# Optimization experiments

Measured on AMD Instinct MI355X. Metric: run time of the kernel, lower is better.

The kernel has to match this reference:

```python
import jax, jax.numpy as jnp
import numpy as np

H, C = 4, 32          # num_heads, hidden_channels
NEG_ATT = 0.2         # GAT attention leaky_relu slope (PyG default)
NEG_ACT = 0.01        # F.leaky_relu default slope applied after each conv


def gat_conv(x_src, x_dst, Wsrc, Wdst, a_src, a_dst, bias, src_idx, dst_idx, n_dst):
    """One bipartite GATConv (add_self_loops=False, concat=True)."""
    hs = (x_src @ Wsrc).reshape(-1, H, C)            # [Ns,H,C]
    hd = (x_dst @ Wdst).reshape(-1, H, C)            # [Nd,H,C]
    a_s = (hs * a_src).sum(-1)                       # [Ns,H]
    a_d = (hd * a_dst).sum(-1)                       # [Nd,H]
    e = jax.nn.leaky_relu(a_s[src_idx] + a_d[dst_idx], NEG_ATT)  # [E,H]
    m = jax.ops.segment_max(e, dst_idx, num_segments=n_dst)      # [Nd,H]
    ex = jnp.exp(e - m[dst_idx])
    denom = jax.ops.segment_sum(ex, dst_idx, num_segments=n_dst)
    alpha = ex / (denom[dst_idx] + 1e-16)            # edge softmax over dst
    msg = hs[src_idx] * alpha[:, :, None]            # [E,H,C]
    out = jax.ops.segment_sum(msg, dst_idx, num_segments=n_dst)  # [Nd,H,C]
    return out.reshape(n_dst, H * C) + bias


def setup_inputs() -> dict:
    key = jax.random.key(0)
    ks = jax.random.split(key, 40)
    it = iter(range(40))
    Nu, Nm, E, D, O = 100000, 20000, 500000, 64, 64
    HC = H * C

    def rn(shape, s=0.1):
        return jax.random.normal(ks[next(it)], shape, jnp.float32) * s

    def ri(n, hi):
        return jax.random.randint(ks[next(it)], (n,), 0, hi)

    return {
        "user_ids": jnp.arange(Nu), "movie_ids": jnp.arange(Nm),
        "um_src": ri(E, Nu), "um_dst": ri(E, Nm),
        "mu_src": ri(E, Nm), "mu_dst": ri(E, Nu),
        "user_emb": rn((Nu, D)), "movie_emb": rn((Nm, D)),
        "l1_um_Wsrc": rn((D, HC)), "l1_um_Wdst": rn((D, HC)),
        "l1_um_asrc": rn((H, C)), "l1_um_adst": rn((H, C)), "l1_um_b": rn((HC,)),
        "l1_mu_Wsrc": rn((D, HC)), "l1_mu_Wdst": rn((D, HC)),
        "l1_mu_asrc": rn((H, C)), "l1_mu_adst": rn((H, C)), "l1_mu_b": rn((HC,)),
        "l2_um_W": rn((HC, HC)), "l2_um_asrc": rn((H, C)), "l2_um_adst": rn((H, C)), "l2_um_b": rn((HC,)),
        "l2_mu_W": rn((HC, HC)), "l2_mu_asrc": rn((H, C)), "l2_mu_adst": rn((H, C)), "l2_mu_b": rn((HC,)),
        "Wo": rn((HC, O)), "bo": rn((O,)),
    }


def reference(user_ids, movie_ids, um_src, um_dst, mu_src, mu_dst,
              user_emb, movie_emb,
              l1_um_Wsrc, l1_um_Wdst, l1_um_asrc, l1_um_adst, l1_um_b,
              l1_mu_Wsrc, l1_mu_Wdst, l1_mu_asrc, l1_mu_adst, l1_mu_b,
              l2_um_W, l2_um_asrc, l2_um_adst, l2_um_b,
              l2_mu_W, l2_mu_asrc, l2_mu_adst, l2_mu_b,
              Wo, bo):
    xu = user_emb[user_ids]
    xm = movie_emb[movie_ids]
    Nu, Nm = xu.shape[0], xm.shape[0]
    # layer 1 (HeteroConv sum: each dst type receives exactly one edge type here)
    hm = gat_conv(xu, xm, l1_um_Wsrc, l1_um_Wdst, l1_um_asrc, l1_um_adst, l1_um_b, um_src, um_dst, Nm)
    hu = gat_conv(xm, xu, l1_mu_Wsrc, l1_mu_Wdst, l1_mu_asrc, l1_mu_adst, l1_mu_b, mu_src, mu_dst, Nu)
    xu = jax.nn.leaky_relu(hu, NEG_ACT)
    xm = jax.nn.leaky_relu(hm, NEG_ACT)
    # layer 2 (non-bipartite in_channels int => shared lin for src and dst)
    hm = gat_conv(xu, xm, l2_um_W, l2_um_W, l2_um_asrc, l2_um_adst, l2_um_b, um_src, um_dst, Nm)
    hu = gat_conv(xm, xu, l2_mu_W, l2_mu_W, l2_mu_asrc, l2_mu_adst, l2_mu_b, mu_src, mu_dst, Nu)
    xu = jax.nn.leaky_relu(hu, NEG_ACT)
    xm = jax.nn.leaky_relu(hm, NEG_ACT)
    out_user = xu @ Wo + bo
    out_movie = xm @ Wo + bo
    return out_user, out_movie, xu, xm
```

## Files before the change

kernel.cpp:

```cpp
#include <hip/hip_runtime.h>
#include <hip/hip_bf16.h>
#include <cstdint>


#define HC 128
#define HH 4
#define NWIN 2

typedef __attribute__((ext_vector_type(8))) short bf16x8;
typedef __attribute__((ext_vector_type(4))) float f32x4;

__device__ __forceinline__ short f2bf(float f) {
    return __builtin_bit_cast(short, __float2bfloat16(f));
}
__device__ __forceinline__ float bf2f(ushort u) {
    return __builtin_bit_cast(float, ((unsigned)u) << 16);
}

struct VT { const float* W[8]; const float* a[8]; float* v[8]; };
__global__ void make_v_all_k(VT t) {
    int gid = blockIdx.x * 256 + threadIdx.x;
    int task, base;
    if (gid < 1024) { task = gid >> 8; base = gid & 255; }
    else if (gid < 3072) { int g = gid - 1024; task = 4 + (g >> 9); base = g & 511; }
    else return;
    int k = base >> 2, h = base & 3;
    int coff = (task & 1) * 4;
    const float* wr = t.W[task] + (size_t)k * HC + h * 32;
    const float* ar = t.a[task] + h * 32;
    float s = 0.f;
    #pragma unroll
    for (int c = 0; c < 32; ++c) s = fmaf(wr[c], ar[c], s);
    t.v[task][k * 8 + coff + h] = s;
}

struct PT { const float* W[5]; const float* V[5]; ushort* Wb[5];
            int K[5]; int Nw[5]; int start[6]; };
__global__ void pack_all_k(PT t) {
    int gid = blockIdx.x * 256 + threadIdx.x;
    if (gid >= t.start[5]) return;
    int task = 0;
    while (gid >= t.start[task + 1]) ++task;
    int loc = gid - t.start[task];
    int K = t.K[task], Nw = t.Nw[task];
    int n = loc / K, k = loc % K;
    float v = 0.f;
    if (n < Nw) v = t.W[task][(size_t)k * Nw + n];
    else if (t.V[task] != nullptr && n < Nw + 8) v = t.V[task][k * 8 + (n - Nw)];
    t.Wb[task][loc] = (ushort)f2bf(v);
}

template <int NT, int MODE, bool ABF>
__global__ __launch_bounds__(256) void gemm_dual_k(
    const void* A0, const int* idx0, const ushort* Wb0, ushort* hsb0,
    ushort* atts0, float* attd0, float* C0, const float* bias0, int M0, int nb0,
    const void* A1, const int* idx1, const ushort* Wb1, ushort* hsb1,
    ushort* atts1, float* attd1, float* C1, const float* bias1, int M1,
    int K, int ldc) {
    const void* A; const int* aidx; const ushort* Wb; ushort* hsb;
    ushort* atts; float* attd; float* C; const float* bias; int M, bid;
    if ((int)blockIdx.x < nb0) {
        A = A0; aidx = idx0; Wb = Wb0; hsb = hsb0; atts = atts0; attd = attd0;
        C = C0; bias = bias0; M = M0; bid = blockIdx.x;
    } else {
        A = A1; aidx = idx1; Wb = Wb1; hsb = hsb1; atts = atts1; attd = attd1;
        C = C1; bias = bias1; M = M1; bid = blockIdx.x - nb0;
    }
    int lane = threadIdx.x & 63;
    int wave = threadIdx.x >> 6;
    int m_base = bid * 128 + wave * 32;
    int lm = lane & 15;
    int kg = lane >> 4;

    int r0 = m_base + lm, r1 = r0 + 16;
    int cr0 = r0 < M ? r0 : M - 1;
    int cr1 = r1 < M ? r1 : M - 1;
    int row0 = aidx ? aidx[cr0] : cr0;
    int row1 = aidx ? aidx[cr1] : cr1;
    const ushort* bp = Wb + (size_t)lm * K + kg * 8;

    f32x4 acc[2][NT] = {};
    for (int k0 = 0; k0 < K; k0 += 32) {
        bf16x8 a[2];
        if (ABF) {
            const ushort* a0p = (const ushort*)A + (size_t)row0 * K + kg * 8;
            const ushort* a1p = (const ushort*)A + (size_t)row1 * K + kg * 8;
            a[0] = *reinterpret_cast<const bf16x8*>(a0p + k0);
            a[1] = *reinterpret_cast<const bf16x8*>(a1p + k0);
        } else {
            const float* a0p = (const float*)A + (size_t)row0 * K + kg * 8;
            const float* a1p = (const float*)A + (size_t)row1 * K + kg * 8;
            float af[2][8];
            *reinterpret_cast<float4*>(&af[0][0]) = *reinterpret_cast<const float4*>(a0p + k0);
            *reinterpret_cast<float4*>(&af[0][4]) = *reinterpret_cast<const float4*>(a0p + k0 + 4);
            *reinterpret_cast<float4*>(&af[1][0]) = *reinterpret_cast<const float4*>(a1p + k0);
            *reinterpret_cast<float4*>(&af[1][4]) = *reinterpret_cast<const float4*>(a1p + k0 + 4);
            #pragma unroll
            for (int mi = 0; mi < 2; ++mi)
                #pragma unroll
                for (int j = 0; j < 8; ++j) a[mi][j] = f2bf(af[mi][j]);
        }
        #pragma unroll
        for (int nt = 0; nt < NT; ++nt) {
            bf16x8 b = *reinterpret_cast<const bf16x8*>(bp + (size_t)nt * 16 * K + k0);
            acc[0][nt] = __builtin_amdgcn_mfma_f32_16x16x32_bf16(a[0], b, acc[0][nt], 0, 0, 0);
            acc[1][nt] = __builtin_amdgcn_mfma_f32_16x16x32_bf16(a[1], b, acc[1][nt], 0, 0, 0);
        }
    }
    #pragma unroll
    for (int mi = 0; mi < 2; ++mi) {
        int rowb = m_base + mi * 16 + kg * 4;
        if (MODE == 0) {
            #pragma unroll
            for (int nt = 0; nt < NT - 1; ++nt) {
                int col = nt * 16 + lm;
                #pragma unroll
                for (int r = 0; r < 4; ++r) {
                    int row = rowb + r;
                    if (row < M) hsb[(size_t)row * HC + col] = (ushort)f2bf(acc[mi][nt][r]);
                }
            }
            #pragma unroll
            for (int r = 0; r < 4; ++r) {
                int row = rowb + r;
                if (row < M) {
                    float v = acc[mi][NT - 1][r];
                    if (lm < 4) atts[(size_t)row * 4 + lm] = (ushort)f2bf(v);
                    else if (lm < 8) attd[(size_t)row * 4 + (lm - 4)] = v;
                }
            }
        } else {
            #pragma unroll
            for (int nt = 0; nt < NT; ++nt) {
                int col = nt * 16 + lm;
                float bv = bias[col];
                #pragma unroll
                for (int r = 0; r < 4; ++r) {
                    int row = rowb + r;
                    if (row < M) C[(size_t)row * ldc + col] = acc[mi][nt][r] + bv;
                }
            }
        }
    }
}

__global__ void hist_dual_k(const int* __restrict__ d0, int* __restrict__ c0, int E0,
                            const int* __restrict__ d1, int* __restrict__ c1, int E1,
                            int* __restrict__ rank) {
    int e = blockIdx.x * 256 + threadIdx.x;
    if (e < E0) rank[e] = atomicAdd(&c0[d0[e]], 1);
    else if (e - E0 < E1) rank[e] = atomicAdd(&c1[d1[e - E0]], 1);
}

__device__ __forceinline__ void scan_block_body(
    const int* deg, int n, int len, int* out, int* partial, int b) {
    __shared__ int s[256];
    int i = b * 256 + threadIdx.x;
    int v = (i < n) ? deg[i] : 0;
    s[threadIdx.x] = v;
    __syncthreads();
    for (int off = 1; off < 256; off <<= 1) {
        int t = (threadIdx.x >= off) ? s[threadIdx.x - off] : 0;
        __syncthreads();
        s[threadIdx.x] += t;
        __syncthreads();
    }
    if (i < len) out[i] = s[threadIdx.x] - v;
    if (threadIdx.x == 255) partial[b] = s[255];
}

__global__ void scan_block_dual_k(const int* dM, int nM, int* rsM, int* pM, int nbM,
                                  const int* dU, int nU, int* rsU, int* pU) {
    if ((int)blockIdx.x < nbM)
        scan_block_body(dM, nM, nM + 1, rsM, pM, blockIdx.x);
    else
        scan_block_body(dU, nU, nU + 1, rsU, pU, blockIdx.x - nbM);
}

__global__ void scan_partial_dual_k(int* pM, int nbM, int* pU, int nbU) {
    __shared__ int s[512];
    int t = threadIdx.x;
    for (int seg = 0; seg < 2; ++seg) {
        int* p = seg ? pU : pM;
        int nb = seg ? nbU : nbM;
        int v = (t < nb) ? p[t] : 0;
        s[t] = v;
        __syncthreads();
        for (int off = 1; off < 512; off <<= 1) {
            int x = (t >= off) ? s[t - off] : 0;
            __syncthreads();
            s[t] += x;
            __syncthreads();
        }
        if (t < nb) p[t] = s[t] - v;
        __syncthreads();
    }
}

__global__ void add_off_dual_k(int* __restrict__ oM, const int* __restrict__ pM,
                               int lenM, int nbM,
                               int* __restrict__ oU, const int* __restrict__ pU,
                               int lenU) {
    int b = blockIdx.x;
    if (b < nbM) {
        int i = b * 256 + threadIdx.x;
        if (i < lenM) oM[i] += pM[b];
    } else {
        b -= nbM;
        int i = b * 256 + threadIdx.x;
        if (i < lenU) oU[i] += pU[b];
    }
}

__global__ void fill_dual_k(const int* __restrict__ s0, const int* __restrict__ d0,
                            const int* __restrict__ rs0, int* __restrict__ csr0,
                            int E0, int n0,
                            const int* __restrict__ s1, const int* __restrict__ d1,
                            const int* __restrict__ rs1, int* __restrict__ csr1,
                            int E1, int n1,
                            const int* __restrict__ rank) {
    int e = blockIdx.x * 256 + threadIdx.x;
    int w = blockIdx.y;
    if (e < E0) {
        int d = d0[e];
        int lo = (int)((long)w * n0 / NWIN), hi = (int)((long)(w + 1) * n0 / NWIN);
        if (d >= lo && d < hi) csr0[rs0[d] + rank[e]] = s0[e];
    } else if (e - E0 < E1) {
        int e1 = e - E0;
        int d = d1[e1];
        int lo = (int)((long)w * n1 / NWIN), hi = (int)((long)(w + 1) * n1 / NWIN);
        if (d >= lo && d < hi) csr1[rs1[d] + rank[e]] = s1[e1];
    }
}

template <bool WF32, bool WBF>
__global__ __launch_bounds__(256) void agg16_dual_k(
    const int* __restrict__ rs0, const int* __restrict__ csr0,
    const ushort* __restrict__ hsb0, const ushort* __restrict__ atts0,
    const float* __restrict__ attd0, const float* __restrict__ bias0,
    float* __restrict__ out0, ushort* __restrict__ outb0, int n0,
    const int* __restrict__ rs1, const int* __restrict__ csr1,
    const ushort* __restrict__ hsb1, const ushort* __restrict__ atts1,
    const float* __restrict__ attd1, const float* __restrict__ bias1,
    float* __restrict__ out1, ushort* __restrict__ outb1, int n1) {
    int g = (int)((blockIdx.x * 256u + threadIdx.x) >> 4);
    const int* rs; const int* csr; const ushort* hsb; const ushort* atts;
    const float* attd; const float* bias; float* out; ushort* outb; int node;
    if (g < n0) {
        rs = rs0; csr = csr0; hsb = hsb0; atts = atts0; attd = attd0;
        bias = bias0; out = out0; outb = outb0; node = g;
    } else {
        node = g - n0;
        if (node >= n1) return;
        rs = rs1; csr = csr1; hsb = hsb1; atts = atts1; attd = attd1;
        bias = bias1; out = out1; outb = outb1;
    }
    int c = threadIdx.x & 15;
    int h = c >> 2;
    float ad = attd[node * 4 + h];
    int s0 = rs[node], s1 = rs[node + 1];
    float acc[8] = {};
    float wsum = 0.f;
    int i = s0;
    for (; i + 4 <= s1; i += 4) {
        int sx[4];
        #pragma unroll
        for (int j = 0; j < 4; ++j) sx[j] = csr[i + j];
        bf16x8 hv[4]; float el[4];
        #pragma unroll
        for (int j = 0; j < 4; ++j) {
            hv[j] = *reinterpret_cast<const bf16x8*>(hsb + (size_t)sx[j] * HC + 8 * c);
            el[j] = bf2f(atts[(size_t)sx[j] * 4 + h]);
        }
        #pragma unroll
        for (int j = 0; j < 4; ++j) {
            float e = el[j] + ad;
            e = e > 0.f ? e : 0.2f * e;
            float w = __expf(e);
            wsum += w;
            #pragma unroll
            for (int k = 0; k < 8; ++k)
                acc[k] = fmaf(w, bf2f((ushort)hv[j][k]), acc[k]);
        }
    }
    for (; i < s1; ++i) {
        int src = csr[i];
        bf16x8 hv = *reinterpret_cast<const bf16x8*>(hsb + (size_t)src * HC + 8 * c);
        float e = bf2f(atts[(size_t)src * 4 + h]) + ad;
        e = e > 0.f ? e : 0.2f * e;
        float w = __expf(e);
        wsum += w;
        #pragma unroll
        for (int k = 0; k < 8; ++k)
            acc[k] = fmaf(w, bf2f((ushort)hv[k]), acc[k]);
    }
    float inv = 1.f / (wsum + 1e-16f);
    float v[8];
    #pragma unroll
    for (int k = 0; k < 8; ++k) {
        v[k] = fmaf(acc[k], inv, bias[8 * c + k]);
        v[k] = v[k] > 0.f ? v[k] : 0.01f * v[k];
    }
    if (WF32) {
        float4 o0 = make_float4(v[0], v[1], v[2], v[3]);
        float4 o1 = make_float4(v[4], v[5], v[6], v[7]);
        reinterpret_cast<float4*>(out + (size_t)node * HC + 8 * c)[0] = o0;
        reinterpret_cast<float4*>(out + (size_t)node * HC + 8 * c)[1] = o1;
    }
    if (WBF) {
        bf16x8 u;
        #pragma unroll
        for (int k = 0; k < 8; ++k) u[k] = f2bf(v[k]);
        *reinterpret_cast<bf16x8*>(outb + (size_t)node * HC + 8 * c) = u;
    }
}

extern "C" void kernel_launch(void* const* d_in, const int* in_sizes, int n_in,
                              void* d_out, int out_size, void* d_ws, size_t ws_size,
                              hipStream_t stream) {
    const int Nu = in_sizes[0];
    const int Nm = in_sizes[1];
    const int E1 = in_sizes[2];
    const int E2 = in_sizes[4];
    const int D  = in_sizes[6] / Nu;
    const int O  = in_sizes[27];

    const int*   user_ids  = (const int*)d_in[0];
    const int*   movie_ids = (const int*)d_in[1];
    const int*   um_src    = (const int*)d_in[2];
    const int*   um_dst    = (const int*)d_in[3];
    const int*   mu_src    = (const int*)d_in[4];
    const int*   mu_dst    = (const int*)d_in[5];
    const float* user_emb  = (const float*)d_in[6];
    const float* movie_emb = (const float*)d_in[7];
    const float* l1_um_Wsrc = (const float*)d_in[8];
    const float* l1_um_Wdst = (const float*)d_in[9];
    const float* l1_um_asrc = (const float*)d_in[10];
    const float* l1_um_adst = (const float*)d_in[11];
    const float* l1_um_b    = (const float*)d_in[12];
    const float* l1_mu_Wsrc = (const float*)d_in[13];
    const float* l1_mu_Wdst = (const float*)d_in[14];
    const float* l1_mu_asrc = (const float*)d_in[15];
    const float* l1_mu_adst = (const float*)d_in[16];
    const float* l1_mu_b    = (const float*)d_in[17];
    const float* l2_um_W    = (const float*)d_in[18];
    const float* l2_um_asrc = (const float*)d_in[19];
    const float* l2_um_adst = (const float*)d_in[20];
    const float* l2_um_b    = (const float*)d_in[21];
    const float* l2_mu_W    = (const float*)d_in[22];
    const float* l2_mu_asrc = (const float*)d_in[23];
    const float* l2_mu_adst = (const float*)d_in[24];
    const float* l2_mu_b    = (const float*)d_in[25];
    const float* Wo         = (const float*)d_in[26];
    const float* bo         = (const float*)d_in[27];

    char* p = (char*)d_ws;
    auto alloc = [&](size_t bytes) { void* r = p; p += (bytes + 255) & ~(size_t)255; return r; };
    ushort* hs_u = (ushort*)alloc((size_t)Nu * HC * 2);
    ushort* hs_m = (ushort*)alloc((size_t)Nm * HC * 2);
    ushort* XUb  = (ushort*)alloc((size_t)Nu * HC * 2);
    ushort* XMb  = (ushort*)alloc((size_t)Nm * HC * 2);
    ushort* atts_u = (ushort*)alloc((size_t)Nu * 4 * 2);
    ushort* atts_m = (ushort*)alloc((size_t)Nm * 4 * 2);
    float* attd_u = (float*)alloc((size_t)Nu * 4 * 4);
    float* attd_m = (float*)alloc((size_t)Nm * 4 * 4);
    float* V_u1  = (float*)alloc((size_t)HC * 8 * 4);
    float* V_m1  = (float*)alloc((size_t)HC * 8 * 4);
    float* V_u2  = (float*)alloc((size_t)HC * 8 * 4);
    float* V_m2  = (float*)alloc((size_t)HC * 8 * 4);
    ushort* Wb_u1 = (ushort*)alloc((size_t)144 * D * 2);
    ushort* Wb_m1 = (ushort*)alloc((size_t)144 * D * 2);
    ushort* Wb_u2 = (ushort*)alloc((size_t)144 * HC * 2);
    ushort* Wb_m2 = (ushort*)alloc((size_t)144 * HC * 2);
    ushort* Wb_o  = (ushort*)alloc((size_t)64 * HC * 2);
    int* um_rs  = (int*)alloc((size_t)(Nm + 1) * 4);
    int* mu_rs  = (int*)alloc((size_t)(Nu + 1) * 4);
    int* cnts   = (int*)alloc((size_t)(Nm + Nu) * 4);
    int* um_cnt = cnts;
    int* mu_cnt = cnts + Nm;
    int* um_csr = (int*)alloc((size_t)E1 * 4);
    int* mu_csr = (int*)alloc((size_t)E2 * 4);
    int* rank   = (int*)alloc((size_t)(E1 + E2) * 4);
    int* partM  = (int*)alloc(512 * 4);
    int* partU  = (int*)alloc(512 * 4);

    auto cdiv = [](int a, int b) { return (a + b - 1) / b; };

    {
        VT vt;
        const float* Ws[8] = {l1_um_Wsrc, l1_mu_Wdst, l1_mu_Wsrc, l1_um_Wdst,
                              l2_um_W, l2_mu_W, l2_mu_W, l2_um_W};
        const float* as[8] = {l1_um_asrc, l1_mu_adst, l1_mu_asrc, l1_um_adst,
                              l2_um_asrc, l2_mu_adst, l2_mu_asrc, l2_um_adst};
        float* vs[8] = {V_u1, V_u1, V_m1, V_m1, V_u2, V_u2, V_m2, V_m2};
        for (int i = 0; i < 8; ++i) { vt.W[i] = Ws[i]; vt.a[i] = as[i]; vt.v[i] = vs[i]; }
        make_v_all_k<<<12, 256, 0, stream>>>(vt);

        PT pt;
        const float* pW[5] = {l1_um_Wsrc, l1_mu_Wsrc, l2_um_W, l2_mu_W, Wo};
        const float* pV[5] = {V_u1, V_m1, V_u2, V_m2, nullptr};
        ushort* pB[5] = {Wb_u1, Wb_m1, Wb_u2, Wb_m2, Wb_o};
        int pK[5] = {D, D, HC, HC, HC};
        int pN[5] = {HC, HC, HC, HC, 64};
        int cum = 0;
        for (int i = 0; i < 5; ++i) {
            pt.W[i] = pW[i]; pt.V[i] = pV[i]; pt.Wb[i] = pB[i];
            pt.K[i] = pK[i]; pt.Nw[i] = pN[i];
            pt.start[i] = cum;
            cum += (i < 4 ? 144 : 64) * pK[i];
        }
        pt.start[5] = cum;
        pack_all_k<<<cdiv(cum, 256), 256, 0, stream>>>(pt);
    }

    int nbM = cdiv(Nm + 1, 256), nbU = cdiv(Nu + 1, 256);
    hipMemsetAsync(cnts, 0, (size_t)(Nm + Nu) * 4, stream);
    hist_dual_k<<<cdiv(E1 + E2, 256), 256, 0, stream>>>(
        um_dst, um_cnt, E1, mu_dst, mu_cnt, E2, rank);
    scan_block_dual_k<<<nbM + nbU, 256, 0, stream>>>(um_cnt, Nm, um_rs, partM, nbM,
                                                     mu_cnt, Nu, mu_rs, partU);
    scan_partial_dual_k<<<1, 512, 0, stream>>>(partM, nbM, partU, nbU);
    add_off_dual_k<<<nbM + nbU, 256, 0, stream>>>(um_rs, partM, Nm + 1, nbM,
                                                  mu_rs, partU, Nu + 1);
    {
        dim3 g(cdiv(E1 + E2, 256), NWIN);
        fill_dual_k<<<g, 256, 0, stream>>>(
            um_src, um_dst, um_rs, um_csr, E1, Nm,
            mu_src, mu_dst, mu_rs, mu_csr, E2, Nu, rank);
    }

    float* OU = (float*)d_out;
    float* OM = OU + (size_t)Nu * O;
    float* XU = OM + (size_t)Nm * O;
    float* XM = XU + (size_t)Nu * HC;

    int gbU = cdiv(Nu, 128), gbM = cdiv(Nm, 128);
    int aggBlocks = cdiv((Nm + Nu) * 16, 256);

    gemm_dual_k<9, 0, false><<<gbU + gbM, 256, 0, stream>>>(
        user_emb, user_ids, Wb_u1, hs_u, atts_u, attd_u, nullptr, nullptr, Nu, gbU,
        movie_emb, movie_ids, Wb_m1, hs_m, atts_m, attd_m, nullptr, nullptr, Nm,
        D, 0);
    agg16_dual_k<false, true><<<aggBlocks, 256, 0, stream>>>(
        um_rs, um_csr, hs_u, atts_u, attd_m, l1_um_b, nullptr, XMb, Nm,
        mu_rs, mu_csr, hs_m, atts_m, attd_u, l1_mu_b, nullptr, XUb, Nu);

    gemm_dual_k<9, 0, true><<<gbU + gbM, 256, 0, stream>>>(
        XUb, nullptr, Wb_u2, hs_u, atts_u, attd_u, nullptr, nullptr, Nu, gbU,
        XMb, nullptr, Wb_m2, hs_m, atts_m, attd_m, nullptr, nullptr, Nm,
        HC, 0);
    agg16_dual_k<true, false><<<aggBlocks, 256, 0, stream>>>(
        um_rs, um_csr, hs_u, atts_u, attd_m, l2_um_b, XM, nullptr, Nm,
        mu_rs, mu_csr, hs_m, atts_m, attd_u, l2_mu_b, XU, nullptr, Nu);

    gemm_dual_k<4, 1, false><<<gbU + gbM, 256, 0, stream>>>(
        XU, nullptr, Wb_o, nullptr, nullptr, nullptr, OU, bo, Nu, gbU,
        XM, nullptr, Wb_o, nullptr, nullptr, nullptr, OM, bo, Nm,
        HC, O);
}
```

Measured before the change: 248.2 us.

## Replace atomic histogram CSR build with two-pass partitioned counting sort

Replaces the global-atomic histogram, per-edge rank and windowed fill with a two-level counting sort over a combined key space of destination nodes. Edges are first bucketed into 512-key partitions using shared-memory counters and a scanned count matrix, then each partition is locally sorted in shared memory to produce row starts and the CSR. The aim is to remove contended global atomics and scattered global writes. The cost is an extra int2 staging buffer, an extra pass over the edges, and a single 256-block final sort kernel that could load-imbalance.

```diff
diff --git a/kernel.cpp b/kernel.cpp
--- a/kernel.cpp
+++ b/kernel.cpp
@@ -5,7 +5,8 @@
 
 #define HC 128
 #define HH 4
-#define NWIN 2
+#define WPART 256
+#define EPB 2048
 
 typedef __attribute__((ext_vector_type(8))) short bf16x8;
 typedef __attribute__((ext_vector_type(4))) float f32x4;
@@ -144,93 +145,124 @@
     }
 }
 
-__global__ void hist_dual_k(const int* __restrict__ d0, int* __restrict__ c0, int E0,
-                            const int* __restrict__ d1, int* __restrict__ c1, int E1,
-                            int* __restrict__ rank) {
-    int e = blockIdx.x * 256 + threadIdx.x;
-    if (e < E0) rank[e] = atomicAdd(&c0[d0[e]], 1);
-    else if (e - E0 < E1) rank[e] = atomicAdd(&c1[d1[e - E0]], 1);
-}
-
-__device__ __forceinline__ void scan_block_body(
-    const int* deg, int n, int len, int* out, int* partial, int b) {
+__global__ __launch_bounds__(256) void part_count_k(
+    const int* __restrict__ d0, int E0,
+    const int* __restrict__ d1, int E1, int Nm,
+    int* __restrict__ cntmat, int NB1) {
+    __shared__ int lh[WPART];
+    int t = threadIdx.x;
+    lh[t] = 0;
+    __syncthreads();
+    int base = blockIdx.x * EPB + t;
+    #pragma unroll
+    for (int j = 0; j < EPB / 256; ++j) {
+        int e = base + j * 256;
+        int key = -1;
+        if (e < E0) key = d0[e];
+        else if (e - E0 < E1) key = Nm + d1[e - E0];
+        if (key >= 0) atomicAdd(&lh[key >> 9], 1);
+    }
+    __syncthreads();
+    cntmat[(size_t)t * NB1 + blockIdx.x] = lh[t];
+}
+
+__global__ __launch_bounds__(256) void part_scatter_k(
+    const int* __restrict__ s0, const int* __restrict__ d0, int E0,
+    const int* __restrict__ s1, const int* __restrict__ d1, int E1, int Nm,
+    const int* __restrict__ scanned, int NB1, int2* __restrict__ buf) {
+    __shared__ int lb[WPART];
+    __shared__ int lc[WPART];
+    int t = threadIdx.x;
+    lb[t] = scanned[(size_t)t * NB1 + blockIdx.x];
+    lc[t] = 0;
+    __syncthreads();
+    int base = blockIdx.x * EPB + t;
+    #pragma unroll
+    for (int j = 0; j < EPB / 256; ++j) {
+        int e = base + j * 256;
+        int key = -1, src = 0;
+        if (e < E0) { key = d0[e]; src = s0[e]; }
+        else if (e - E0 < E1) { key = Nm + d1[e - E0]; src = s1[e - E0]; }
+        if (key >= 0) {
+            int w = key >> 9;
+            int r = atomicAdd(&lc[w], 1);
+            buf[lb[w] + r] = make_int2(src, key);
+        }
+    }
+}
+
+__global__ __launch_bounds__(512) void csort_k(
+    const int2* __restrict__ buf, const int* __restrict__ scanned, int NB1,
+    int E, int NK, int* __restrict__ rs, int* __restrict__ csr) {
+    __shared__ int c1[512];
+    __shared__ int ls[512];
+    int b = blockIdx.x;
+    int t = threadIdx.x;
+    int lo = scanned[(size_t)b * NB1];
+    int hi = (b + 1 < WPART) ? scanned[(size_t)(b + 1) * NB1] : E;
+    int keylo = b << 9;
+    c1[t] = 0;
+    __syncthreads();
+    for (int i = lo + t; i < hi; i += 512)
+        atomicAdd(&c1[buf[i].y - keylo], 1);
+    __syncthreads();
+    int v = c1[t];
+    ls[t] = v;
+    __syncthreads();
+    for (int off = 1; off < 512; off <<= 1) {
+        int x = (t >= off) ? ls[t - off] : 0;
+        __syncthreads();
+        ls[t] += x;
+        __syncthreads();
+    }
+    ls[t] -= v;
+    int gk = keylo + t;
+    if (gk <= NK) rs[gk] = lo + ls[t];
+    c1[t] = 0;
+    __syncthreads();
+    for (int i = lo + t; i < hi; i += 512) {
+        int2 p = buf[i];
+        int k = p.y - keylo;
+        int r = atomicAdd(&c1[k], 1);
+        csr[lo + ls[k] + r] = p.x;
+    }
+}
+
+__global__ void scan_block_k(const int* __restrict__ deg, int n,
+                             int* __restrict__ out, int* __restrict__ partial) {
     __shared__ int s[256];
-    int i = b * 256 + threadIdx.x;
+    int i = blockIdx.x * 256 + threadIdx.x;
     int v = (i < n) ? deg[i] : 0;
     s[threadIdx.x] = v;
     __syncthreads();
     for (int off = 1; off < 256; off <<= 1) {
-        int t = (threadIdx.x >= off) ? s[threadIdx.x - off] : 0;
-        __syncthreads();
-        s[threadIdx.x] += t;
-        __syncthreads();
-    }
-    if (i < len) out[i] = s[threadIdx.x] - v;
-    if (threadIdx.x == 255) partial[b] = s[255];
-}
-
-__global__ void scan_block_dual_k(const int* dM, int nM, int* rsM, int* pM, int nbM,
-                                  const int* dU, int nU, int* rsU, int* pU) {
-    if ((int)blockIdx.x < nbM)
-        scan_block_body(dM, nM, nM + 1, rsM, pM, blockIdx.x);
-    else
-        scan_block_body(dU, nU, nU + 1, rsU, pU, blockIdx.x - nbM);
-}
-
-__global__ void scan_partial_dual_k(int* pM, int nbM, int* pU, int nbU) {
+        int x = (threadIdx.x >= off) ? s[threadIdx.x - off] : 0;
+        __syncthreads();
+        s[threadIdx.x] += x;
+        __syncthreads();
+    }
+    if (i < n) out[i] = s[threadIdx.x] - v;
+    if (threadIdx.x == 255) partial[blockIdx.x] = s[255];
+}
+
+__global__ void scan_partial_k(int* __restrict__ partial, int nb) {
     __shared__ int s[512];
     int t = threadIdx.x;
-    for (int seg = 0; seg < 2; ++seg) {
-        int* p = seg ? pU : pM;
-        int nb = seg ? nbU : nbM;
-        int v = (t < nb) ? p[t] : 0;
-        s[t] = v;
-        __syncthreads();
-        for (int off = 1; off < 512; off <<= 1) {
-            int x = (t >= off) ? s[t - off] : 0;
-            __syncthreads();
-            s[t] += x;
-            __syncthreads();
-        }
-        if (t < nb) p[t] = s[t] - v;
-        __syncthreads();
-    }
-}
-
-__global__ void add_off_dual_k(int* __restrict__ oM, const int* __restrict__ pM,
-                               int lenM, int nbM,
-                               int* __restrict__ oU, const int* __restrict__ pU,
-                               int lenU) {
-    int b = blockIdx.x;
-    if (b < nbM) {
-        int i = b * 256 + threadIdx.x;
-        if (i < lenM) oM[i] += pM[b];
-    } else {
-        b -= nbM;
-        int i = b * 256 + threadIdx.x;
-        if (i < lenU) oU[i] += pU[b];
-    }
-}
-
-__global__ void fill_dual_k(const int* __restrict__ s0, const int* __restrict__ d0,
-                            const int* __restrict__ rs0, int* __restrict__ csr0,
-                            int E0, int n0,
-                            const int* __restrict__ s1, const int* __restrict__ d1,
-                            const int* __restrict__ rs1, int* __restrict__ csr1,
-                            int E1, int n1,
-                            const int* __restrict__ rank) {
-    int e = blockIdx.x * 256 + threadIdx.x;
-    int w = blockIdx.y;
-    if (e < E0) {
-        int d = d0[e];
-        int lo = (int)((long)w * n0 / NWIN), hi = (int)((long)(w + 1) * n0 / NWIN);
-        if (d >= lo && d < hi) csr0[rs0[d] + rank[e]] = s0[e];
-    } else if (e - E0 < E1) {
-        int e1 = e - E0;
-        int d = d1[e1];
-        int lo = (int)((long)w * n1 / NWIN), hi = (int)((long)(w + 1) * n1 / NWIN);
-        if (d >= lo && d < hi) csr1[rs1[d] + rank[e]] = s1[e1];
-    }
+    int v = (t < nb) ? partial[t] : 0;
+    s[t] = v;
+    __syncthreads();
+    for (int off = 1; off < 512; off <<= 1) {
+        int x = (t >= off) ? s[t - off] : 0;
+        __syncthreads();
+        s[t] += x;
+        __syncthreads();
+    }
+    if (t < nb) partial[t] = s[t] - v;
+}
+
+__global__ void add_off_k(int* __restrict__ out, const int* __restrict__ partial, int n) {
+    int i = blockIdx.x * 256 + threadIdx.x;
+    if (i < n) out[i] += partial[blockIdx.x];
 }
 
 template <bool WF32, bool WBF>
@@ -324,6 +356,8 @@
     const int E2 = in_sizes[4];
     const int D  = in_sizes[6] / Nu;
     const int O  = in_sizes[27];
+    const int E  = E1 + E2;
+    const int NK = Nm + Nu;
 
     const int*   user_ids  = (const int*)d_in[0];
     const int*   movie_ids = (const int*)d_in[1];
@@ -354,6 +388,10 @@
     const float* Wo         = (const float*)d_in[26];
     const float* bo         = (const float*)d_in[27];
 
+    auto cdiv = [](int a, int b) { return (a + b - 1) / b; };
+    const int NB1 = cdiv(E, EPB);
+    const int CM  = WPART * NB1;
+
     char* p = (char*)d_ws;
     auto alloc = [&](size_t bytes) { void* r = p; p += (bytes + 255) & ~(size_t)255; return r; };
     ushort* hs_u = (ushort*)alloc((size_t)Nu * HC * 2);
@@ -373,18 +411,12 @@
     ushort* Wb_u2 = (ushort*)alloc((size_t)144 * HC * 2);
     ushort* Wb_m2 = (ushort*)alloc((size_t)144 * HC * 2);
     ushort* Wb_o  = (ushort*)alloc((size_t)64 * HC * 2);
-    int* um_rs  = (int*)alloc((size_t)(Nm + 1) * 4);
-    int* mu_rs  = (int*)alloc((size_t)(Nu + 1) * 4);
-    int* cnts   = (int*)alloc((size_t)(Nm + Nu) * 4);
-    int* um_cnt = cnts;
-    int* mu_cnt = cnts + Nm;
-    int* um_csr = (int*)alloc((size_t)E1 * 4);
-    int* mu_csr = (int*)alloc((size_t)E2 * 4);
-    int* rank   = (int*)alloc((size_t)(E1 + E2) * 4);
-    int* partM  = (int*)alloc(512 * 4);
-    int* partU  = (int*)alloc(512 * 4);
-
-    auto cdiv = [](int a, int b) { return (a + b - 1) / b; };
+    int* rs      = (int*)alloc((size_t)(NK + 2) * 4);
+    int* cntmat  = (int*)alloc((size_t)(CM + 256) * 4);
+    int* scanned = (int*)alloc((size_t)(CM + 256) * 4);
+    int2* buf    = (int2*)alloc((size_t)E * 8);
+    int* csr     = (int*)alloc((size_t)E * 4);
+    int* part    = (int*)alloc(1024 * 4);
 
     {
         VT vt;
@@ -413,21 +445,16 @@
         pack_all_k<<<cdiv(cum, 256), 256, 0, stream>>>(pt);
     }
 
-    int nbM = cdiv(Nm + 1, 256), nbU = cdiv(Nu + 1, 256);
-    hipMemsetAsync(cnts, 0, (size_t)(Nm + Nu) * 4, stream);
-    hist_dual_k<<<cdiv(E1 + E2, 256), 256, 0, stream>>>(
-        um_dst, um_cnt, E1, mu_dst, mu_cnt, E2, rank);
-    scan_block_dual_k<<<nbM + nbU, 256, 0, stream>>>(um_cnt, Nm, um_rs, partM, nbM,
-                                                     mu_cnt, Nu, mu_rs, partU);
-    scan_partial_dual_k<<<1, 512, 0, stream>>>(partM, nbM, partU, nbU);
-    add_off_dual_k<<<nbM + nbU, 256, 0, stream>>>(um_rs, partM, Nm + 1, nbM,
-                                                  mu_rs, partU, Nu + 1);
+    part_count_k<<<NB1, 256, 0, stream>>>(um_dst, E1, mu_dst, E2, Nm, cntmat, NB1);
     {
-        dim3 g(cdiv(E1 + E2, 256), NWIN);
-        fill_dual_k<<<g, 256, 0, stream>>>(
-            um_src, um_dst, um_rs, um_csr, E1, Nm,
-            mu_src, mu_dst, mu_rs, mu_csr, E2, Nu, rank);
-    }
+        int nb = cdiv(CM, 256);
+        scan_block_k<<<nb, 256, 0, stream>>>(cntmat, CM, scanned, part);
+        scan_partial_k<<<1, 512, 0, stream>>>(part, nb);
+        add_off_k<<<nb, 256, 0, stream>>>(scanned, part, CM);
+    }
+    part_scatter_k<<<NB1, 256, 0, stream>>>(um_src, um_dst, E1, mu_src, mu_dst, E2,
+                                            Nm, scanned, NB1, buf);
+    csort_k<<<WPART, 512, 0, stream>>>(buf, scanned, NB1, E, NK, rs, csr);
 
     float* OU = (float*)d_out;
     float* OM = OU + (size_t)Nu * O;
@@ -442,16 +469,16 @@
         movie_emb, movie_ids, Wb_m1, hs_m, atts_m, attd_m, nullptr, nullptr, Nm,
         D, 0);
     agg16_dual_k<false, true><<<aggBlocks, 256, 0, stream>>>(
-        um_rs, um_csr, hs_u, atts_u, attd_m, l1_um_b, nullptr, XMb, Nm,
-        mu_rs, mu_csr, hs_m, atts_m, attd_u, l1_mu_b, nullptr, XUb, Nu);
+        rs, csr, hs_u, atts_u, attd_m, l1_um_b, nullptr, XMb, Nm,
+        rs + Nm, csr, hs_m, atts_m, attd_u, l1_mu_b, nullptr, XUb, Nu);
 
     gemm_dual_k<9, 0, true><<<gbU + gbM, 256, 0, stream>>>(
         XUb, nullptr, Wb_u2, hs_u, atts_u, attd_u, nullptr, nullptr, Nu, gbU,
         XMb, nullptr, Wb_m2, hs_m, atts_m, attd_m, nullptr, nullptr, Nm,
         HC, 0);
     agg16_dual_k<true, false><<<aggBlocks, 256, 0, stream>>>(
-        um_rs, um_csr, hs_u, atts_u, attd_m, l2_um_b, XM, nullptr, Nm,
-        mu_rs, mu_csr, hs_m, atts_m, attd_u, l2_mu_b, XU, nullptr, Nu);
+        rs, csr, hs_u, atts_u, attd_m, l2_um_b, XM, nullptr, Nm,
+        rs + Nm, csr, hs_m, atts_m, attd_u, l2_mu_b, XU, nullptr, Nu);
 
     gemm_dual_k<4, 1, false><<<gbU + gbM, 256, 0, stream>>>(
         XU, nullptr, Wb_o, nullptr, nullptr, nullptr, OU, bo, Nu, gbU,
```

After: 213.6 us. 1.16x faster.
